# Performance work log

Hardware: AMD Instinct MI355X
Metric: run time of the kernel (lower is better)

Reference implementation:

```python
import jax, jax.numpy as jnp
import numpy as np

N_NODES = 50000
N_EDGES = 1600000
C_IN = 128
H = 128
NEG_SLOPE = 0.01  # torch LeakyReLU default
BN_EPS = 1e-5


def setup_inputs() -> dict:
    key = jax.random.key(0)
    ks = jax.random.split(key, 10)
    x = jax.random.normal(ks[0], (N_NODES, C_IN), dtype=jnp.float32)
    edge_index = jax.random.randint(ks[1], (2, N_EDGES), 0, N_NODES, dtype=jnp.int64)
    batch = jnp.zeros((N_NODES,), dtype=jnp.int64)
    # GraphConv params: lin_rel (with bias) applied to aggregated neighbors,
    # lin_root (no bias) applied to self features. Xavier-uniform scale.
    def xavier(k, shape):
        fan_in, fan_out = shape[1], shape[0]
        lim = float(np.sqrt(6.0 / (fan_in + fan_out)))
        return jax.random.uniform(k, shape, jnp.float32, -lim, lim)
    W_rel = xavier(ks[2], (H, C_IN))
    b_rel = jnp.zeros((H,), dtype=jnp.float32)
    W_root = xavier(ks[3], (H, C_IN))
    W_lin = xavier(ks[4], (H, H))
    b_lin = jnp.zeros((H,), dtype=jnp.float32)
    gamma = jnp.ones((H,), dtype=jnp.float32)
    beta = jnp.zeros((H,), dtype=jnp.float32)
    return {"x": x, "edge_index": edge_index, "batch": batch,
            "W_rel": W_rel, "b_rel": b_rel, "W_root": W_root,
            "W_lin": W_lin, "b_lin": b_lin, "gamma": gamma, "beta": beta}


def leaky_relu(v):
    return jnp.where(v >= 0, v, NEG_SLOPE * v)


def reference(x, edge_index, batch, W_rel, b_rel, W_root, W_lin, b_lin, gamma, beta):
    src, dst = edge_index[0], edge_index[1]
    # GraphConv with 'add' aggregation: gather source features, scatter-add to dst.
    agg = jax.ops.segment_sum(x[src], dst, num_segments=x.shape[0])  # [N, C_IN]
    x1 = agg @ W_rel.T + b_rel + x @ W_root.T                        # [N, H]
    x2 = leaky_relu(x1)
    x3 = x2 @ W_lin.T + b_lin
    # BatchNorm1d (training mode): biased batch statistics over nodes.
    mean = jnp.mean(x3, axis=0)
    var = jnp.mean(jnp.square(x3 - mean), axis=0)
    x4 = (x3 - mean) * jax.lax.rsqrt(var + BN_EPS) * gamma + beta
    return leaky_relu(x4)
```

## Files before the change

kernel.cpp:

```cpp
#include <hip/hip_runtime.h>

#define NNODES 50000
#define NEG 0.01f
#define BN_EPS 1e-5f

#define BINSZ 64
#define NBINS 782
#define CAPG 4096
#define PH1B 256
#define RING 32

typedef __attribute__((ext_vector_type(8))) short bf16x8;
typedef __attribute__((ext_vector_type(4))) float f32x4;

__device__ __forceinline__ float lrelu(float v) { return v >= 0.f ? v : NEG * v; }
__device__ __forceinline__ float bf_lo(unsigned u) { return __uint_as_float(u << 16); }
__device__ __forceinline__ float bf_hi(unsigned u) { return __uint_as_float(u & 0xffff0000u); }
__device__ __forceinline__ unsigned f2bf(float x) {
    unsigned u = __float_as_uint(x);
    return (u + 0x7fffu + ((u >> 16) & 1u)) >> 16;
}
__device__ __forceinline__ unsigned packbf(float lo, float hi) {
    unsigned b = __float_as_uint(hi);
    b = (b + 0x7fffu + ((b >> 16) & 1u)) & 0xffff0000u;
    return (f2bf(lo) & 0xffffu) | b;
}
__device__ __forceinline__ void acc8(float* c, uint4 q) {
    c[0] += bf_lo(q.x); c[1] += bf_hi(q.x);
    c[2] += bf_lo(q.y); c[3] += bf_hi(q.y);
    c[4] += bf_lo(q.z); c[5] += bf_hi(q.z);
    c[6] += bf_lo(q.w); c[7] += bf_hi(q.w);
}

__global__ __launch_bounds__(256)
void prep_kernel(const float* __restrict__ x, const float* __restrict__ Wrel,
                 const float* __restrict__ Wroot, const float* __restrict__ Wlin,
                 unsigned* __restrict__ xb2, unsigned* __restrict__ wb2)
{
    const int NPX = 3200000;
    const int NPW = 24576;
    for (int i = blockIdx.x * 256 + threadIdx.x; i < NPX + NPW; i += gridDim.x * 256) {
        if (i < NPX) {
            float2 v = ((const float2*)x)[i];
            xb2[i] = packbf(v.x, v.y);
        } else {
            int j = i - NPX;
            const float* W = (j < 8192) ? Wrel : (j < 16384 ? Wroot : Wlin);
            float2 v = ((const float2*)W)[j & 8191];
            wb2[j] = packbf(v.x, v.y);
        }
    }
}

__global__ __launch_bounds__(256)
void bin_kernel(const int* __restrict__ src, const int* __restrict__ dst,
                int* __restrict__ bcnt, unsigned* __restrict__ recs, int n_edges)
{
    __shared__ __align__(16) unsigned buf[NBINS][RING];
    __shared__ int cnt[NBINS];
    __shared__ int flushed[NBINS];

    const int tid = threadIdx.x;
    for (int t = tid; t < NBINS; t += 256) { cnt[t] = 0; flushed[t] = 0; }
    __syncthreads();

    const int per = (n_edges + PH1B - 1) / PH1B;
    const int begin = blockIdx.x * per;
    const int end = min(begin + per, n_edges);

    for (int base = begin; base < end; base += 256) {
        int i = base + tid;
        if (i < end) {
            int s = src[i], d = dst[i];
            int b = d >> 6;
            unsigned rec = (unsigned)s | ((unsigned)(d & 63) << 16);
            int pos = atomicAdd(&cnt[b], 1);
            buf[b][pos & (RING - 1)] = rec;
        }
        __syncthreads();
        for (int t = tid; t < NBINS; t += 256) {
            int c = cnt[t];
            int f = flushed[t];
            while (c - f >= 16) {
                int gbase = atomicAdd(&bcnt[t], 16);
                unsigned* dp = recs + (long)t * CAPG + gbase;
                int ro = f & (RING - 1);
                #pragma unroll
                for (int k = 0; k < 4; ++k)
                    *(uint4*)(dp + k * 4) = *(uint4*)&buf[t][ro + k * 4];
                f += 16;
            }
            flushed[t] = f;
        }
        __syncthreads();
    }
    for (int t = tid; t < NBINS; t += 256) {
        int c = cnt[t], f = flushed[t];
        int n = c - f;
        if (n > 0) {
            int gbase = atomicAdd(&bcnt[t], n);
            unsigned* dp = recs + (long)t * CAPG + gbase;
            int ro = f & (RING - 1);
            for (int k = 0; k < n; ++k) dp[k] = buf[t][ro + k];
        }
    }
}

__global__ __launch_bounds__(512, 6)
void agg_mlp_kernel(const unsigned* __restrict__ xb2, const unsigned* __restrict__ recs,
                    const int* __restrict__ bcnt, const unsigned short* __restrict__ wb,
                    const float* __restrict__ brel, const float* __restrict__ blin,
                    float* __restrict__ out, float* __restrict__ sums,
                    float* __restrict__ sumsq)
{
    __shared__ unsigned srec[CAPG];
    __shared__ int cnt[BINSZ];
    __shared__ int pos[BINSZ];
    __shared__ int offs[BINSZ + 1];
    __shared__ __align__(16) unsigned short smA[BINSZ][136];

    const int bin = blockIdx.x;
    const int tid = threadIdx.x;
    const int l = tid & 63, w = tid >> 6;
    const int l15 = l & 15, kg = l >> 4;
    const int g16 = l >> 4, c16 = l & 15;

    if (tid < BINSZ) cnt[tid] = 0;
    __syncthreads();

    const int n = bcnt[bin];
    const unsigned* rp = recs + (long)bin * CAPG;

    for (int i = tid; i < n; i += 512)
        atomicAdd(&cnt[(rp[i] >> 16) & 63], 1);
    __syncthreads();

    if (tid < 64) {
        int v = cnt[tid];
        int inc = v;
        #pragma unroll
        for (int d = 1; d < 64; d <<= 1) {
            int u = __shfl_up(inc, d);
            if (tid >= d) inc += u;
        }
        offs[tid] = inc - v;
        pos[tid] = inc - v;
        if (tid == 63) offs[64] = inc;
    }
    __syncthreads();

    for (int i = tid; i < n; i += 512) {
        unsigned r = rp[i];
        int p = atomicAdd(&pos[(r >> 16) & 63], 1);
        srec[p] = r;
    }
    __syncthreads();

    unsigned* smA32 = (unsigned*)smA;
    for (int lo = w; lo < BINSZ; lo += 8) {
        const int b = offs[lo], e = offs[lo + 1];
        float c[8];
        #pragma unroll
        for (int k = 0; k < 8; ++k) c[k] = 0.f;

        int i = b;
        for (; i + 16 <= e; i += 16) {
            unsigned r0 = srec[i + g16];
            unsigned r1 = srec[i + 4 + g16];
            unsigned r2 = srec[i + 8 + g16];
            unsigned r3 = srec[i + 12 + g16];
            uint4 q0 = *((const uint4*)(xb2 + (r0 & 0xffffu) * 64) + c16);
            uint4 q1 = *((const uint4*)(xb2 + (r1 & 0xffffu) * 64) + c16);
            uint4 q2 = *((const uint4*)(xb2 + (r2 & 0xffffu) * 64) + c16);
            uint4 q3 = *((const uint4*)(xb2 + (r3 & 0xffffu) * 64) + c16);
            acc8(c, q0); acc8(c, q1); acc8(c, q2); acc8(c, q3);
        }
        for (; i + 4 <= e; i += 4) {
            unsigned r = srec[i + g16];
            uint4 q = *((const uint4*)(xb2 + (r & 0xffffu) * 64) + c16);
            acc8(c, q);
        }
        if (i < e) {
            int idx = i + g16;
            unsigned r = srec[idx < e ? idx : e - 1];
            if (idx < e) {
                uint4 q = *((const uint4*)(xb2 + (r & 0xffffu) * 64) + c16);
                acc8(c, q);
            }
        }
        #pragma unroll
        for (int k = 0; k < 8; ++k) {
            c[k] += __shfl_xor(c[k], 16);
            c[k] += __shfl_xor(c[k], 32);
        }
        if (l < 16) {
            uint4 o;
            o.x = packbf(c[0], c[1]); o.y = packbf(c[2], c[3]);
            o.z = packbf(c[4], c[5]); o.w = packbf(c[6], c[7]);
            *((uint4*)(smA32 + lo * 68) + c16) = o;
        }
    }
    __syncthreads();

    const unsigned short* Wrelb  = wb;
    const unsigned short* Wrootb = wb + 16384;
    const unsigned short* Wlinb  = wb + 32768;
    const unsigned short* xbs = (const unsigned short*)xb2;

    const int m  = w & 3;
    const int ch = w >> 2;
    const int row = m * 16 + l15;
    const int gA = bin * 64 + row;
    const long gAc = min(gA, NNODES - 1);

    f32x4 acc[4];
    #pragma unroll
    for (int nt = 0; nt < 4; ++nt) acc[nt] = (f32x4){0.f, 0.f, 0.f, 0.f};

    #pragma unroll
    for (int s = 0; s < 8; ++s) {
        const int ko = (s & 3) * 32 + kg * 8;
        bf16x8 a;
        if (s < 4) a = *(const bf16x8*)&smA[row][ko];
        else       a = *(const bf16x8*)(xbs + gAc * 128 + ko);
        const unsigned short* Bb = (s < 4) ? Wrelb : Wrootb;
        #pragma unroll
        for (int nt = 0; nt < 4; ++nt) {
            bf16x8 b = *(const bf16x8*)(Bb + (ch * 64 + nt * 16 + l15) * 128 + ko);
            acc[nt] = __builtin_amdgcn_mfma_f32_16x16x32_bf16(a, b, acc[nt], 0, 0, 0);
        }
    }
    __syncthreads();

    #pragma unroll
    for (int nt = 0; nt < 4; ++nt) {
        const int col = ch * 64 + nt * 16 + l15;
        const float br = brel[col];
        #pragma unroll
        for (int r = 0; r < 4; ++r) {
            smA[m * 16 + kg * 4 + r][col] =
                (unsigned short)f2bf(lrelu(acc[nt][r] + br));
        }
    }
    __syncthreads();

    f32x4 acc2[4];
    #pragma unroll
    for (int nt = 0; nt < 4; ++nt) acc2[nt] = (f32x4){0.f, 0.f, 0.f, 0.f};

    #pragma unroll
    for (int s = 0; s < 4; ++s) {
        const int ko = s * 32 + kg * 8;
        bf16x8 a = *(const bf16x8*)&smA[row][ko];
        #pragma unroll
        for (int nt = 0; nt < 4; ++nt) {
            bf16x8 b = *(const bf16x8*)(Wlinb + (ch * 64 + nt * 16 + l15) * 128 + ko);
            acc2[nt] = __builtin_amdgcn_mfma_f32_16x16x32_bf16(a, b, acc2[nt], 0, 0, 0);
        }
    }

    float* redS = (float*)srec;
    #pragma unroll
    for (int nt = 0; nt < 4; ++nt) {
        const int col = ch * 64 + nt * 16 + l15;
        const float bl = blin[col];
        float ps = 0.f, pq = 0.f;
        #pragma unroll
        for (int r = 0; r < 4; ++r) {
            int g = bin * 64 + m * 16 + kg * 4 + r;
            if (g < NNODES) {
                float y = acc2[nt][r] + bl;
                out[(long)g * 128 + col] = y;
                ps += y; pq += y * y;
            }
        }
        ps += __shfl_xor(ps, 16); ps += __shfl_xor(ps, 32);
        pq += __shfl_xor(pq, 16); pq += __shfl_xor(pq, 32);
        if (kg == 0) {
            redS[(0 * 4 + m) * 128 + col] = ps;
            redS[(1 * 4 + m) * 128 + col] = pq;
        }
    }
    __syncthreads();
    if (tid < 128) {
        float s = redS[0 * 128 + tid] + redS[1 * 128 + tid]
                + redS[2 * 128 + tid] + redS[3 * 128 + tid];
        float q = redS[4 * 128 + tid] + redS[5 * 128 + tid]
                + redS[6 * 128 + tid] + redS[7 * 128 + tid];
        atomicAdd(&sums[tid], s);
        atomicAdd(&sumsq[tid], q);
    }
}

__global__ void bn_final_kernel(const float* __restrict__ sums, const float* __restrict__ sumsq,
                                const float* __restrict__ gamma, const float* __restrict__ beta,
                                float* __restrict__ ss)
{
    int h = threadIdx.x;
    float mean = sums[h] * (1.f / NNODES);
    float var = sumsq[h] * (1.f / NNODES) - mean * mean;
    float sc = gamma[h] * rsqrtf(var + BN_EPS);
    ss[h] = sc;
    ss[128 + h] = beta[h] - mean * sc;
}

__global__ __launch_bounds__(256)
void bn_apply_kernel(float* __restrict__ out, const float* __restrict__ ss)
{
    __shared__ float s_sc[128], s_sh[128];
    if (threadIdx.x < 128) {
        s_sc[threadIdx.x] = ss[threadIdx.x];
        s_sh[threadIdx.x] = ss[128 + threadIdx.x];
    }
    __syncthreads();
    const int total = NNODES * 32;
    float4* o4 = (float4*)out;
    for (int i = blockIdx.x * 256 + threadIdx.x; i < total; i += gridDim.x * 256) {
        float4 v = o4[i];
        int h = (i & 31) * 4;
        v.x = lrelu(v.x * s_sc[h + 0] + s_sh[h + 0]);
        v.y = lrelu(v.y * s_sc[h + 1] + s_sh[h + 1]);
        v.z = lrelu(v.z * s_sc[h + 2] + s_sh[h + 2]);
        v.w = lrelu(v.w * s_sc[h + 3] + s_sh[h + 3]);
        o4[i] = v;
    }
}

extern "C" void kernel_launch(void* const* d_in, const int* in_sizes, int n_in,
                              void* d_out, int out_size, void* d_ws, size_t ws_size,
                              hipStream_t stream)
{
    const float* x     = (const float*)d_in[0];
    const int*   ei    = (const int*)d_in[1];
    const float* Wrel  = (const float*)d_in[3];
    const float* brel  = (const float*)d_in[4];
    const float* Wroot = (const float*)d_in[5];
    const float* Wlin  = (const float*)d_in[6];
    const float* blin  = (const float*)d_in[7];
    const float* gamma = (const float*)d_in[8];
    const float* beta  = (const float*)d_in[9];
    float* out = (float*)d_out;

    const int n_edges = in_sizes[1] / 2;
    const int* src = ei;
    const int* dst = ei + n_edges;

    char* ws = (char*)d_ws;
    unsigned short* xb   = (unsigned short*)ws;
    unsigned*       recs = (unsigned*)(ws + 12800000);
    unsigned short* wb   = (unsigned short*)(ws + 25612288);
    int*   bcnt  = (int*)(ws + 25710592);
    float* sums  = (float*)(ws + 25713792);
    float* sumsq = sums + 128;
    float* ss    = sums + 256;

    hipMemsetAsync(bcnt, 0, 5248, stream);

    prep_kernel<<<4096, 256, 0, stream>>>(x, Wrel, Wroot, Wlin, (unsigned*)xb, (unsigned*)wb);
    bin_kernel<<<PH1B, 256, 0, stream>>>(src, dst, bcnt, recs, n_edges);
    agg_mlp_kernel<<<NBINS, 512, 0, stream>>>((const unsigned*)xb, recs, bcnt, wb,
                                              brel, blin, out, sums, sumsq);
    bn_final_kernel<<<1, 128, 0, stream>>>(sums, sumsq, gamma, beta, ss);
    bn_apply_kernel<<<2048, 256, 0, stream>>>(out, ss);
}
```

Baseline: 164.1 us.

## Sort bin edges by source-node tile to improve gather locality

```diff
diff --git a/kernel.cpp b/kernel.cpp
--- a/kernel.cpp
+++ b/kernel.cpp
@@ -9,6 +9,8 @@
 #define CAPG 4096
 #define PH1B 256
 #define RING 32
+#define NTILE 7
+#define NKEY (NTILE * 64)
 
 typedef __attribute__((ext_vector_type(8))) short bf16x8;
 typedef __attribute__((ext_vector_type(4))) float f32x4;
@@ -106,18 +108,21 @@
     }
 }
 
-__global__ __launch_bounds__(512, 6)
+__global__ __launch_bounds__(512, 3)
 void agg_mlp_kernel(const unsigned* __restrict__ xb2, const unsigned* __restrict__ recs,
                     const int* __restrict__ bcnt, const unsigned short* __restrict__ wb,
                     const float* __restrict__ brel, const float* __restrict__ blin,
                     float* __restrict__ out, float* __restrict__ sums,
                     float* __restrict__ sumsq)
 {
-    __shared__ unsigned srec[CAPG];
-    __shared__ int cnt[BINSZ];
-    __shared__ int pos[BINSZ];
-    __shared__ int offs[BINSZ + 1];
-    __shared__ __align__(16) unsigned short smA[BINSZ][136];
+    __shared__ __align__(16) char poolA[32768];
+    __shared__ __align__(16) char poolB[21768];
+
+    float*    accf = (float*)poolA;
+    unsigned* srec = (unsigned*)poolB;
+    int*      cnt  = (int*)(poolB + 16384);
+    int*      pos  = (int*)(poolB + 18176);
+    int*      offs = (int*)(poolB + 19968);
 
     const int bin = blockIdx.x;
     const int tid = threadIdx.x;
@@ -125,80 +130,100 @@
     const int l15 = l & 15, kg = l >> 4;
     const int g16 = l >> 4, c16 = l & 15;
 
-    if (tid < BINSZ) cnt[tid] = 0;
+    for (int k = tid; k < NKEY; k += 512) cnt[k] = 0;
+    #pragma unroll
+    for (int i = 0; i < 4; ++i)
+        *(float4*)&accf[(tid + i * 512) * 4] = make_float4(0.f, 0.f, 0.f, 0.f);
     __syncthreads();
 
     const int n = bcnt[bin];
     const unsigned* rp = recs + (long)bin * CAPG;
 
-    for (int i = tid; i < n; i += 512)
-        atomicAdd(&cnt[(rp[i] >> 16) & 63], 1);
-    __syncthreads();
-
-    if (tid < 64) {
-        int v = cnt[tid];
-        int inc = v;
-        #pragma unroll
-        for (int d = 1; d < 64; d <<= 1) {
-            int u = __shfl_up(inc, d);
-            if (tid >= d) inc += u;
-        }
-        offs[tid] = inc - v;
-        pos[tid] = inc - v;
-        if (tid == 63) offs[64] = inc;
-    }
-    __syncthreads();
-
     for (int i = tid; i < n; i += 512) {
         unsigned r = rp[i];
-        int p = atomicAdd(&pos[(r >> 16) & 63], 1);
+        int key = (int)((r & 0xffffu) >> 13) * 64 + (int)((r >> 16) & 63);
+        atomicAdd(&cnt[key], 1);
+    }
+    __syncthreads();
+
+    if (w == 0) {
+        int carry = 0;
+        for (int base = 0; base < NKEY; base += 64) {
+            int v = cnt[base + l];
+            int inc = v;
+            #pragma unroll
+            for (int d = 1; d < 64; d <<= 1) {
+                int u = __shfl_up(inc, d);
+                if (l >= d) inc += u;
+            }
+            offs[base + l] = carry + inc - v;
+            pos[base + l]  = carry + inc - v;
+            carry += __shfl(inc, 63);
+        }
+        if (l == 0) offs[NKEY] = carry;
+    }
+    __syncthreads();
+
+    for (int i = tid; i < n; i += 512) {
+        unsigned r = rp[i];
+        int key = (int)((r & 0xffffu) >> 13) * 64 + (int)((r >> 16) & 63);
+        int p = atomicAdd(&pos[key], 1);
         srec[p] = r;
     }
     __syncthreads();
 
-    unsigned* smA32 = (unsigned*)smA;
-    for (int lo = w; lo < BINSZ; lo += 8) {
-        const int b = offs[lo], e = offs[lo + 1];
-        float c[8];
-        #pragma unroll
-        for (int k = 0; k < 8; ++k) c[k] = 0.f;
-
-        int i = b;
-        for (; i + 16 <= e; i += 16) {
-            unsigned r0 = srec[i + g16];
-            unsigned r1 = srec[i + 4 + g16];
-            unsigned r2 = srec[i + 8 + g16];
-            unsigned r3 = srec[i + 12 + g16];
-            uint4 q0 = *((const uint4*)(xb2 + (r0 & 0xffffu) * 64) + c16);
-            uint4 q1 = *((const uint4*)(xb2 + (r1 & 0xffffu) * 64) + c16);
-            uint4 q2 = *((const uint4*)(xb2 + (r2 & 0xffffu) * 64) + c16);
-            uint4 q3 = *((const uint4*)(xb2 + (r3 & 0xffffu) * 64) + c16);
-            acc8(c, q0); acc8(c, q1); acc8(c, q2); acc8(c, q3);
-        }
-        for (; i + 4 <= e; i += 4) {
-            unsigned r = srec[i + g16];
-            uint4 q = *((const uint4*)(xb2 + (r & 0xffffu) * 64) + c16);
-            acc8(c, q);
-        }
-        if (i < e) {
-            int idx = i + g16;
-            unsigned r = srec[idx < e ? idx : e - 1];
-            if (idx < e) {
+    for (int t = 0; t < NTILE; ++t) {
+        #pragma unroll
+        for (int di = 0; di < 8; ++di) {
+            const int d = w + 8 * di;
+            const int key = t * 64 + d;
+            const int b = offs[key], e = offs[key + 1];
+            if (b >= e) continue;
+            float c[8];
+            #pragma unroll
+            for (int k = 0; k < 8; ++k) c[k] = 0.f;
+
+            int i = b;
+            for (; i + 4 <= e; i += 4) {
+                unsigned r = srec[i + g16];
                 uint4 q = *((const uint4*)(xb2 + (r & 0xffffu) * 64) + c16);
                 acc8(c, q);
             }
-        }
-        #pragma unroll
-        for (int k = 0; k < 8; ++k) {
-            c[k] += __shfl_xor(c[k], 16);
-            c[k] += __shfl_xor(c[k], 32);
-        }
-        if (l < 16) {
-            uint4 o;
-            o.x = packbf(c[0], c[1]); o.y = packbf(c[2], c[3]);
-            o.z = packbf(c[4], c[5]); o.w = packbf(c[6], c[7]);
-            *((uint4*)(smA32 + lo * 68) + c16) = o;
-        }
+            if (i < e) {
+                int idx = i + g16;
+                if (idx < e) {
+                    unsigned r = srec[idx];
+                    uint4 q = *((const uint4*)(xb2 + (r & 0xffffu) * 64) + c16);
+                    acc8(c, q);
+                }
+            }
+            #pragma unroll
+            for (int k = 0; k < 8; ++k) {
+                c[k] += __shfl_xor(c[k], 16);
+                c[k] += __shfl_xor(c[k], 32);
+            }
+            if (l < 16) {
+                float* ap = accf + d * 128 + c16 * 8;
+                float4 v0 = *(float4*)ap;
+                float4 v1 = *(float4*)(ap + 4);
+                v0.x += c[0]; v0.y += c[1]; v0.z += c[2]; v0.w += c[3];
+                v1.x += c[4]; v1.y += c[5]; v1.z += c[6]; v1.w += c[7];
+                *(float4*)ap = v0;
+                *(float4*)(ap + 4) = v1;
+            }
+        }
+    }
+    __syncthreads();
+
+    unsigned short (*smA)[136] = (unsigned short (*)[136])poolB;
+    unsigned* smA32 = (unsigned*)poolB;
+    #pragma unroll
+    for (int it = 0; it < 8; ++it) {
+        int idx = tid + it * 512;
+        int node = idx >> 6, cu = idx & 63;
+        float f0 = accf[node * 128 + cu * 2];
+        float f1 = accf[node * 128 + cu * 2 + 1];
+        smA32[node * 68 + cu] = packbf(f0, f1);
     }
     __syncthreads();
 
@@ -259,7 +284,7 @@
         }
     }
 
-    float* redS = (float*)srec;
+    float* redS = (float*)poolA;
     #pragma unroll
     for (int nt = 0; nt < 4; ++nt) {
         const int col = ch * 64 + nt * 16 + l15;
```

Result: slower. 234.9 us (+43.1%).

## Split neighbor gather into four column-quarter passes with 16 edges per wave

Applied to the files above, without the earlier changes.

```diff
diff --git a/kernel.cpp b/kernel.cpp
--- a/kernel.cpp
+++ b/kernel.cpp
@@ -106,7 +106,7 @@
     }
 }
 
-__global__ __launch_bounds__(512, 6)
+__global__ __launch_bounds__(512, 4)
 void agg_mlp_kernel(const unsigned* __restrict__ xb2, const unsigned* __restrict__ recs,
                     const int* __restrict__ bcnt, const unsigned short* __restrict__ wb,
                     const float* __restrict__ brel, const float* __restrict__ blin,
@@ -123,7 +123,7 @@
     const int tid = threadIdx.x;
     const int l = tid & 63, w = tid >> 6;
     const int l15 = l & 15, kg = l >> 4;
-    const int g16 = l >> 4, c16 = l & 15;
+    const int g4 = l >> 2, c4 = l & 3;
 
     if (tid < BINSZ) cnt[tid] = 0;
     __syncthreads();
@@ -157,47 +157,36 @@
     __syncthreads();
 
     unsigned* smA32 = (unsigned*)smA;
-    for (int lo = w; lo < BINSZ; lo += 8) {
-        const int b = offs[lo], e = offs[lo + 1];
-        float c[8];
-        #pragma unroll
-        for (int k = 0; k < 8; ++k) c[k] = 0.f;
-
-        int i = b;
-        for (; i + 16 <= e; i += 16) {
-            unsigned r0 = srec[i + g16];
-            unsigned r1 = srec[i + 4 + g16];
-            unsigned r2 = srec[i + 8 + g16];
-            unsigned r3 = srec[i + 12 + g16];
-            uint4 q0 = *((const uint4*)(xb2 + (r0 & 0xffffu) * 64) + c16);
-            uint4 q1 = *((const uint4*)(xb2 + (r1 & 0xffffu) * 64) + c16);
-            uint4 q2 = *((const uint4*)(xb2 + (r2 & 0xffffu) * 64) + c16);
-            uint4 q3 = *((const uint4*)(xb2 + (r3 & 0xffffu) * 64) + c16);
-            acc8(c, q0); acc8(c, q1); acc8(c, q2); acc8(c, q3);
-        }
-        for (; i + 4 <= e; i += 4) {
-            unsigned r = srec[i + g16];
-            uint4 q = *((const uint4*)(xb2 + (r & 0xffffu) * 64) + c16);
-            acc8(c, q);
-        }
-        if (i < e) {
-            int idx = i + g16;
-            unsigned r = srec[idx < e ? idx : e - 1];
-            if (idx < e) {
-                uint4 q = *((const uint4*)(xb2 + (r & 0xffffu) * 64) + c16);
-                acc8(c, q);
-            }
-        }
-        #pragma unroll
-        for (int k = 0; k < 8; ++k) {
-            c[k] += __shfl_xor(c[k], 16);
-            c[k] += __shfl_xor(c[k], 32);
-        }
-        if (l < 16) {
-            uint4 o;
-            o.x = packbf(c[0], c[1]); o.y = packbf(c[2], c[3]);
-            o.z = packbf(c[4], c[5]); o.w = packbf(c[6], c[7]);
-            *((uint4*)(smA32 + lo * 68) + c16) = o;
+    for (int q = 0; q < 4; ++q) {
+        #pragma unroll
+        for (int di = 0; di < 8; ++di) {
+            const int d = w + 8 * di;
+            const int b = offs[d], e = offs[d + 1];
+            float c[8];
+            #pragma unroll
+            for (int k = 0; k < 8; ++k) c[k] = 0.f;
+
+            for (int i = b; i < e; i += 16) {
+                int idx = i + g4;
+                if (idx < e) {
+                    unsigned r = srec[idx];
+                    uint4 qv = *((const uint4*)(xb2 + (r & 0xffffu) * 64 + q * 16) + c4);
+                    acc8(c, qv);
+                }
+            }
+            #pragma unroll
+            for (int k = 0; k < 8; ++k) {
+                c[k] += __shfl_xor(c[k], 4);
+                c[k] += __shfl_xor(c[k], 8);
+                c[k] += __shfl_xor(c[k], 16);
+                c[k] += __shfl_xor(c[k], 32);
+            }
+            if (l < 4) {
+                uint4 o;
+                o.x = packbf(c[0], c[1]); o.y = packbf(c[2], c[3]);
+                o.z = packbf(c[4], c[5]); o.w = packbf(c[6], c[7]);
+                *((uint4*)(smA32 + d * 68 + q * 16) + c4) = o;
+            }
         }
     }
     __syncthreads();
```

Result: slower. 195.3 us (+19.0%).

## Fuse bf16 prep into binning kernel and fold BN finalize into apply

Applied to the files above, without the earlier changes.

```diff
diff --git a/kernel.cpp b/kernel.cpp
--- a/kernel.cpp
+++ b/kernel.cpp
@@ -9,6 +9,10 @@
 #define CAPG 4096
 #define PH1B 256
 #define RING 32
+
+#define NPX 3200000
+#define NPW 24576
+#define NPAIR (NPX + NPW)
 
 typedef __attribute__((ext_vector_type(8))) short bf16x8;
 typedef __attribute__((ext_vector_type(4))) float f32x4;
@@ -33,28 +37,11 @@
 }
 
 __global__ __launch_bounds__(256)
-void prep_kernel(const float* __restrict__ x, const float* __restrict__ Wrel,
-                 const float* __restrict__ Wroot, const float* __restrict__ Wlin,
-                 unsigned* __restrict__ xb2, unsigned* __restrict__ wb2)
-{
-    const int NPX = 3200000;
-    const int NPW = 24576;
-    for (int i = blockIdx.x * 256 + threadIdx.x; i < NPX + NPW; i += gridDim.x * 256) {
-        if (i < NPX) {
-            float2 v = ((const float2*)x)[i];
-            xb2[i] = packbf(v.x, v.y);
-        } else {
-            int j = i - NPX;
-            const float* W = (j < 8192) ? Wrel : (j < 16384 ? Wroot : Wlin);
-            float2 v = ((const float2*)W)[j & 8191];
-            wb2[j] = packbf(v.x, v.y);
-        }
-    }
-}
-
-__global__ __launch_bounds__(256)
-void bin_kernel(const int* __restrict__ src, const int* __restrict__ dst,
-                int* __restrict__ bcnt, unsigned* __restrict__ recs, int n_edges)
+void prep_bin_kernel(const float* __restrict__ x, const float* __restrict__ Wrel,
+                     const float* __restrict__ Wroot, const float* __restrict__ Wlin,
+                     unsigned* __restrict__ xb2, unsigned* __restrict__ wb2,
+                     const int* __restrict__ src, const int* __restrict__ dst,
+                     int* __restrict__ bcnt, unsigned* __restrict__ recs, int n_edges)
 {
     __shared__ __align__(16) unsigned buf[NBINS][RING];
     __shared__ int cnt[NBINS];
@@ -68,7 +55,29 @@
     const int begin = blockIdx.x * per;
     const int end = min(begin + per, n_edges);
 
+    const int pper = (NPAIR + PH1B - 1) / PH1B;
+    const int pbegin = blockIdx.x * pper;
+    const int pend = min(pbegin + pper, NPAIR);
+    int pi = 0;
+
     for (int base = begin; base < end; base += 256) {
+        #pragma unroll
+        for (int k = 0; k < 2; ++k) {
+            int i = pbegin + pi + k * 256 + tid;
+            if (i < pend) {
+                if (i < NPX) {
+                    float2 v = ((const float2*)x)[i];
+                    xb2[i] = packbf(v.x, v.y);
+                } else {
+                    int j = i - NPX;
+                    const float* W = (j < 8192) ? Wrel : (j < 16384 ? Wroot : Wlin);
+                    float2 v = ((const float2*)W)[j & 8191];
+                    wb2[j] = packbf(v.x, v.y);
+                }
+            }
+        }
+        pi += 512;
+
         int i = base + tid;
         if (i < end) {
             int s = src[i], d = dst[i];
@@ -94,6 +103,17 @@
         }
         __syncthreads();
     }
+    for (int i = pbegin + pi + tid; i < pend; i += 256) {
+        if (i < NPX) {
+            float2 v = ((const float2*)x)[i];
+            xb2[i] = packbf(v.x, v.y);
+        } else {
+            int j = i - NPX;
+            const float* W = (j < 8192) ? Wrel : (j < 16384 ? Wroot : Wlin);
+            float2 v = ((const float2*)W)[j & 8191];
+            wb2[j] = packbf(v.x, v.y);
+        }
+    }
     for (int t = tid; t < NBINS; t += 256) {
         int c = cnt[t], f = flushed[t];
         int n = c - f;
@@ -182,8 +202,8 @@
         }
         if (i < e) {
             int idx = i + g16;
-            unsigned r = srec[idx < e ? idx : e - 1];
             if (idx < e) {
+                unsigned r = srec[idx];
                 uint4 q = *((const uint4*)(xb2 + (r & 0xffffu) * 64) + c16);
                 acc8(c, q);
             }
@@ -292,25 +312,19 @@
     }
 }
 
-__global__ void bn_final_kernel(const float* __restrict__ sums, const float* __restrict__ sumsq,
-                                const float* __restrict__ gamma, const float* __restrict__ beta,
-                                float* __restrict__ ss)
-{
-    int h = threadIdx.x;
-    float mean = sums[h] * (1.f / NNODES);
-    float var = sumsq[h] * (1.f / NNODES) - mean * mean;
-    float sc = gamma[h] * rsqrtf(var + BN_EPS);
-    ss[h] = sc;
-    ss[128 + h] = beta[h] - mean * sc;
-}
-
 __global__ __launch_bounds__(256)
-void bn_apply_kernel(float* __restrict__ out, const float* __restrict__ ss)
+void bn_apply_kernel(float* __restrict__ out,
+                     const float* __restrict__ sums, const float* __restrict__ sumsq,
+                     const float* __restrict__ gamma, const float* __restrict__ beta)
 {
     __shared__ float s_sc[128], s_sh[128];
     if (threadIdx.x < 128) {
-        s_sc[threadIdx.x] = ss[threadIdx.x];
-        s_sh[threadIdx.x] = ss[128 + threadIdx.x];
+        int h = threadIdx.x;
+        float mean = sums[h] * (1.f / NNODES);
+        float var = sumsq[h] * (1.f / NNODES) - mean * mean;
+        float sc = gamma[h] * rsqrtf(var + BN_EPS);
+        s_sc[h] = sc;
+        s_sh[h] = beta[h] - mean * sc;
     }
     __syncthreads();
     const int total = NNODES * 32;
@@ -352,14 +366,13 @@
     int*   bcnt  = (int*)(ws + 25710592);
     float* sums  = (float*)(ws + 25713792);
     float* sumsq = sums + 128;
-    float* ss    = sums + 256;
 
     hipMemsetAsync(bcnt, 0, 5248, stream);
 
-    prep_kernel<<<4096, 256, 0, stream>>>(x, Wrel, Wroot, Wlin, (unsigned*)xb, (unsigned*)wb);
-    bin_kernel<<<PH1B, 256, 0, stream>>>(src, dst, bcnt, recs, n_edges);
+    prep_bin_kernel<<<PH1B, 256, 0, stream>>>(x, Wrel, Wroot, Wlin,
+                                              (unsigned*)xb, (unsigned*)wb,
+                                              src, dst, bcnt, recs, n_edges);
     agg_mlp_kernel<<<NBINS, 512, 0, stream>>>((const unsigned*)xb, recs, bcnt, wb,
                                               brel, blin, out, sums, sumsq);
-    bn_final_kernel<<<1, 128, 0, stream>>>(sums, sumsq, gamma, beta, ss);
-    bn_apply_kernel<<<2048, 256, 0, stream>>>(out, ss);
-}
+    bn_apply_kernel<<<2048, 256, 0, stream>>>(out, sums, sumsq, gamma, beta);
+}
```

Result: slower. 168.8 us (+2.9%).
